# Performance work log

Measured on AMD Instinct MI355X. Metric: run time of the kernel, lower is better.

Reference implementation:

```python
import jax, jax.numpy as jnp
import numpy as np

T, B, D, H = 1024, 8, 1024, 16
HD = D // H  # head_dim = 64


def setup_inputs() -> dict:
    key = jax.random.key(0)
    ks = jax.random.split(key, 11)
    s = 1.0 / np.sqrt(D)
    return {
        "query": jax.random.normal(ks[0], (T, B, D), jnp.float32),
        "key": jax.random.normal(ks[1], (T, B, D), jnp.float32),
        "value": jax.random.normal(ks[2], (T, B, D), jnp.float32),
        "Wq": jax.random.normal(ks[3], (D, D), jnp.float32) * s,
        "bq": jax.random.normal(ks[4], (D,), jnp.float32) * s,
        "Wk": jax.random.normal(ks[5], (D, D), jnp.float32) * s,
        "bk": jax.random.normal(ks[6], (D,), jnp.float32) * s,
        "Wv": jax.random.normal(ks[7], (D, D), jnp.float32) * s,
        "bv": jax.random.normal(ks[8], (D,), jnp.float32) * s,
        "Wo": jax.random.normal(ks[9], (D, D), jnp.float32) * s,
        "bo": jax.random.normal(ks[10], (D,), jnp.float32) * s,
    }


def reference(query, key, value, Wq, bq, Wk, bk, Wv, bv, Wo, bo):
    # query/key/value: (T, B, D) seq-first, as in nn.MultiheadAttention
    t, b, d = query.shape
    scale = HD ** -0.5
    # projections (torch Linear: x @ W.T + b), split into heads -> (B, H, T, HD)
    q = (query @ Wq.T + bq).reshape(t, b, H, HD).transpose(1, 2, 0, 3)
    k = (key @ Wk.T + bk).reshape(t, b, H, HD).transpose(1, 2, 0, 3)
    v = (value @ Wv.T + bv).reshape(t, b, H, HD).transpose(1, 2, 0, 3)
    # full (B, H, T, T) scores, matching the module's explicit materialization
    attn = jnp.einsum('bhtd,bhsd->bhts', q, k) * scale
    attn = jax.nn.softmax(attn, axis=-1)
    # (B, H, T, HD) -> (T, B, D)
    out = jnp.einsum('bhts,bhsd->bhtd', attn, v)
    out = out.transpose(2, 0, 1, 3).reshape(t, b, d)
    return out @ Wo.T + bo
```

## Files before the change

kernel.cpp:

```cpp
#include <hip/hip_runtime.h>

#define T_SEQ 1024
#define BATCH 8
#define DMODEL 1024
#define NHEAD 16
#define HDIM 64
#define M_ROWS (T_SEQ * BATCH)

typedef unsigned short ushort_t;
typedef __attribute__((ext_vector_type(8))) short short8;
typedef __attribute__((ext_vector_type(4))) float f32x4;

#define G2L16(g, l) __builtin_amdgcn_global_load_lds(                      \
    (const __attribute__((address_space(1))) void*)(g),                    \
    (__attribute__((address_space(3))) void*)(l), 16, 0, 0)

static __device__ __forceinline__ ushort_t f2bf(float f) {
    unsigned int u = __builtin_bit_cast(unsigned int, f);
    u += 0x7FFFu + ((u >> 16) & 1u);
    return (ushort_t)(u >> 16);
}

__global__ __launch_bounds__(256) void cast_bf16(const float4* __restrict__ in,
                                                 uint2* __restrict__ out, int n4) {
    int i = blockIdx.x * 256 + threadIdx.x;
    if (i < n4) {
        float4 v = in[i];
        uint2 o;
        o.x = (unsigned)f2bf(v.x) | ((unsigned)f2bf(v.y) << 16);
        o.y = (unsigned)f2bf(v.z) | ((unsigned)f2bf(v.w) << 16);
        out[i] = o;
    }
}

template<bool OUT_BF16>
__global__ __launch_bounds__(256) void gemm_bt_mfma(
    const ushort_t* __restrict__ A, const ushort_t* __restrict__ Wb,
    const float* __restrict__ bias, void* __restrict__ Yv,
    int M, int N, int K, float scale)
{
    __shared__ ushort_t As[128 * 32];
    __shared__ ushort_t Bs[128 * 32];

    const int tid  = threadIdx.x;
    const int lane = tid & 63;
    const int quad = lane >> 4;
    const int l16  = lane & 15;
    const int w    = tid >> 6;
    const int wm   = w >> 1;
    const int wn   = w & 1;
    const int bn   = blockIdx.x;
    const int bm   = blockIdx.y;

    const int srow_in = lane >> 2;
    const int sch     = lane & 3;

    const f32x4 zero4 = {0.f, 0.f, 0.f, 0.f};
    f32x4 acc[4][4];
#pragma unroll
    for (int i = 0; i < 4; i++)
#pragma unroll
        for (int j = 0; j < 4; j++) acc[i][j] = zero4;

    const int fswz = (l16 >> 1) & 3;

    for (int k0 = 0; k0 < K; k0 += 32) {
        __syncthreads();
#pragma unroll
        for (int u = 0; u < 2; u++) {
            int seg = w * 2 + u;
            int row = seg * 16 + srow_in;
            int chs = sch ^ ((row >> 1) & 3);
            G2L16(&A [(size_t)(bm * 128 + row) * K + k0 + chs * 8],
                  (char*)As + seg * 1024);
            G2L16(&Wb[(size_t)(bn * 128 + row) * K + k0 + chs * 8],
                  (char*)Bs + seg * 1024);
        }
        __syncthreads();

        short8 af[4], bfr[4];
#pragma unroll
        for (int i = 0; i < 4; i++) {
            int row = wm * 64 + i * 16 + l16;
            af[i] = *(const short8*)&As[row * 32 + (quad ^ fswz) * 8];
        }
#pragma unroll
        for (int j = 0; j < 4; j++) {
            int row = wn * 64 + j * 16 + l16;
            bfr[j] = *(const short8*)&Bs[row * 32 + (quad ^ fswz) * 8];
        }
#pragma unroll
        for (int i = 0; i < 4; i++)
#pragma unroll
            for (int j = 0; j < 4; j++)
                acc[i][j] = __builtin_amdgcn_mfma_f32_16x16x32_bf16(
                    af[i], bfr[j], acc[i][j], 0, 0, 0);
    }

    float bj[4];
#pragma unroll
    for (int j = 0; j < 4; j++) bj[j] = bias[bn * 128 + wn * 64 + j * 16 + l16];
#pragma unroll
    for (int i = 0; i < 4; i++) {
#pragma unroll
        for (int r = 0; r < 4; r++) {
            size_t row = (size_t)(bm * 128 + wm * 64 + i * 16 + quad * 4 + r);
#pragma unroll
            for (int j = 0; j < 4; j++) {
                int col = bn * 128 + wn * 64 + j * 16 + l16;
                float v = (acc[i][j][r] + bj[j]) * scale;
                if (OUT_BF16) ((ushort_t*)Yv)[row * N + col] = f2bf(v);
                else          ((float*)   Yv)[row * N + col] = v;
            }
        }
    }
}

__global__ __launch_bounds__(256) void transpose_v(
    const ushort_t* __restrict__ Vp, ushort_t* __restrict__ Vt)
{
    __shared__ ushort_t Ts[64][72];
    const int tid = threadIdx.x;
    const int t0 = blockIdx.x * 64;
    const int bh = blockIdx.y;
    const int b = bh >> 4, h = bh & 15;

#pragma unroll
    for (int u = 0; u < 2; u++) {
        int e = u * 256 + tid;
        int row = e >> 3, ch = (e & 7) * 8;
        uint4 v = *(const uint4*)&Vp[((size_t)(t0 + row) * BATCH + b) * DMODEL + h * 64 + ch];
        *(uint4*)&Ts[row][ch] = v;
    }
    __syncthreads();
#pragma unroll
    for (int u = 0; u < 2; u++) {
        int e = u * 256 + tid;
        int d = e >> 3, tc = (e & 7) * 8;
        uint4 o;
        o.x = (unsigned)Ts[tc + 0][d] | ((unsigned)Ts[tc + 1][d] << 16);
        o.y = (unsigned)Ts[tc + 2][d] | ((unsigned)Ts[tc + 3][d] << 16);
        o.z = (unsigned)Ts[tc + 4][d] | ((unsigned)Ts[tc + 5][d] << 16);
        o.w = (unsigned)Ts[tc + 6][d] | ((unsigned)Ts[tc + 7][d] << 16);
        *(uint4*)&Vt[((size_t)(bh * 64 + d)) * T_SEQ + t0 + tc] = o;
    }
}

__global__ __launch_bounds__(256) void attn_mfma(
    const ushort_t* __restrict__ Qp, const ushort_t* __restrict__ Kp,
    const ushort_t* __restrict__ VtG, ushort_t* __restrict__ Ao)
{
    __shared__ ushort_t Ks[64 * 64];
    __shared__ ushort_t Vs[64 * 64];
    __shared__ ushort_t Pl[4][32][72];

    const int tid  = threadIdx.x;
    const int lane = tid & 63;
    const int w    = tid >> 6;
    const int quad = lane >> 4;
    const int l16  = lane & 15;
    const int bid  = blockIdx.x;
    const int qb   = bid >> 7;
    const int bh   = bid & 127;
    const int b    = bh >> 4, h = bh & 15;
    const int hoff = h * 64;
    const int q0   = qb * 128 + w * 32;

    const int srow_in = lane >> 3;
    const int sch     = lane & 7;

    short8 qf[2][2];
#pragma unroll
    for (int rt = 0; rt < 2; rt++)
#pragma unroll
        for (int ks = 0; ks < 2; ks++)
            qf[rt][ks] = *(const short8*)&Qp[((size_t)(q0 + rt * 16 + l16) * BATCH + b) * DMODEL
                                             + hoff + ks * 32 + quad * 8];

    short8 ones;
#pragma unroll
    for (int i = 0; i < 8; i++) ones[i] = (short)0x3F80;

    const f32x4 zero4 = {0.f, 0.f, 0.f, 0.f};
    f32x4 oacc[2][4], lacc[2];
#pragma unroll
    for (int rt = 0; rt < 2; rt++) {
        lacc[rt] = zero4;
#pragma unroll
        for (int c = 0; c < 4; c++) oacc[rt][c] = zero4;
    }

    for (int s0 = 0; s0 < T_SEQ; s0 += 64) {
        __syncthreads();
#pragma unroll
        for (int u = 0; u < 2; u++) {
            int seg = w * 2 + u;
            int row = seg * 8 + srow_in;
            int chs = sch ^ (row & 7);
            G2L16(&Kp[((size_t)(s0 + row) * BATCH + b) * DMODEL + hoff + chs * 8],
                  (char*)Ks + seg * 1024);
            G2L16(&VtG[((size_t)(bh * 64 + row)) * T_SEQ + s0 + chs * 8],
                  (char*)Vs + seg * 1024);
        }
        __syncthreads();

        f32x4 sacc[2][4];
#pragma unroll
        for (int rt = 0; rt < 2; rt++)
#pragma unroll
            for (int c = 0; c < 4; c++) sacc[rt][c] = zero4;
#pragma unroll
        for (int c = 0; c < 4; c++) {
            int row = c * 16 + l16;
#pragma unroll
            for (int ks = 0; ks < 2; ks++) {
                short8 kf = *(const short8*)&Ks[row * 64 + (((ks * 4 + quad) ^ (row & 7)) * 8)];
#pragma unroll
                for (int rt = 0; rt < 2; rt++)
                    sacc[rt][c] = __builtin_amdgcn_mfma_f32_16x16x32_bf16(
                        qf[rt][ks], kf, sacc[rt][c], 0, 0, 0);
            }
        }

#pragma unroll
        for (int rt = 0; rt < 2; rt++)
#pragma unroll
            for (int c = 0; c < 4; c++)
#pragma unroll
                for (int r = 0; r < 4; r++)
                    Pl[w][rt * 16 + quad * 4 + r][c * 16 + l16] =
                        f2bf(__expf(sacc[rt][c][r]));

        short8 pf[2][2];
#pragma unroll
        for (int rt = 0; rt < 2; rt++)
#pragma unroll
            for (int ks = 0; ks < 2; ks++)
                pf[rt][ks] = *(const short8*)&Pl[w][rt * 16 + l16][ks * 32 + quad * 8];

#pragma unroll
        for (int rt = 0; rt < 2; rt++)
#pragma unroll
            for (int ks = 0; ks < 2; ks++)
                lacc[rt] = __builtin_amdgcn_mfma_f32_16x16x32_bf16(
                    pf[rt][ks], ones, lacc[rt], 0, 0, 0);

#pragma unroll
        for (int dt = 0; dt < 4; dt++) {
            int row = dt * 16 + l16;
#pragma unroll
            for (int ks = 0; ks < 2; ks++) {
                short8 vf = *(const short8*)&Vs[row * 64 + (((ks * 4 + quad) ^ (row & 7)) * 8)];
#pragma unroll
                for (int rt = 0; rt < 2; rt++)
                    oacc[rt][dt] = __builtin_amdgcn_mfma_f32_16x16x32_bf16(
                        pf[rt][ks], vf, oacc[rt][dt], 0, 0, 0);
            }
        }
    }

#pragma unroll
    for (int rt = 0; rt < 2; rt++)
#pragma unroll
        for (int r = 0; r < 4; r++) {
            float inv = 1.f / lacc[rt][r];
            size_t t = (size_t)(q0 + rt * 16 + quad * 4 + r);
#pragma unroll
            for (int c = 0; c < 4; c++)
                Ao[(t * BATCH + b) * DMODEL + hoff + c * 16 + l16] =
                    f2bf(oacc[rt][c][r] * inv);
        }
}

extern "C" void kernel_launch(void* const* d_in, const int* in_sizes, int n_in,
                              void* d_out, int out_size, void* d_ws, size_t ws_size,
                              hipStream_t stream)
{
    const float* q  = (const float*)d_in[0];
    const float* k  = (const float*)d_in[1];
    const float* v  = (const float*)d_in[2];
    const float* Wq = (const float*)d_in[3];
    const float* bq = (const float*)d_in[4];
    const float* Wk = (const float*)d_in[5];
    const float* bk = (const float*)d_in[6];
    const float* Wv = (const float*)d_in[7];
    const float* bv = (const float*)d_in[8];
    const float* Wo = (const float*)d_in[9];
    const float* bo = (const float*)d_in[10];

    ushort_t* ws = (ushort_t*)d_ws;
    const size_t E = (size_t)M_ROWS * DMODEL;
    const size_t EW = (size_t)DMODEL * DMODEL;
    ushort_t* qb  = ws;
    ushort_t* kb  = ws + E;
    ushort_t* vb  = ws + 2 * E;
    ushort_t* Qp  = ws + 3 * E;
    ushort_t* Kp  = ws + 4 * E;
    ushort_t* Vp  = ws + 5 * E;
    ushort_t* Wqb = ws + 6 * E;
    ushort_t* Wkb = Wqb + EW;
    ushort_t* Wvb = Wkb + EW;
    ushort_t* Wob = Wvb + EW;
    ushort_t* Vt  = qb;
    ushort_t* Aob = kb;

    const int n4_in = (int)(E / 4);
    const int n4_w  = (int)(EW / 4);
    cast_bf16<<<n4_in / 256, 256, 0, stream>>>((const float4*)q,  (uint2*)qb,  n4_in);
    cast_bf16<<<n4_in / 256, 256, 0, stream>>>((const float4*)k,  (uint2*)kb,  n4_in);
    cast_bf16<<<n4_in / 256, 256, 0, stream>>>((const float4*)v,  (uint2*)vb,  n4_in);
    cast_bf16<<<n4_w  / 256, 256, 0, stream>>>((const float4*)Wq, (uint2*)Wqb, n4_w);
    cast_bf16<<<n4_w  / 256, 256, 0, stream>>>((const float4*)Wk, (uint2*)Wkb, n4_w);
    cast_bf16<<<n4_w  / 256, 256, 0, stream>>>((const float4*)Wv, (uint2*)Wvb, n4_w);
    cast_bf16<<<n4_w  / 256, 256, 0, stream>>>((const float4*)Wo, (uint2*)Wob, n4_w);

    dim3 gg(DMODEL / 128, M_ROWS / 128);
    gemm_bt_mfma<true><<<gg, 256, 0, stream>>>(qb, Wqb, bq, Qp, M_ROWS, DMODEL, DMODEL, 0.125f);
    gemm_bt_mfma<true><<<gg, 256, 0, stream>>>(kb, Wkb, bk, Kp, M_ROWS, DMODEL, DMODEL, 1.0f);
    gemm_bt_mfma<true><<<gg, 256, 0, stream>>>(vb, Wvb, bv, Vp, M_ROWS, DMODEL, DMODEL, 1.0f);

    transpose_v<<<dim3(T_SEQ / 64, BATCH * NHEAD), 256, 0, stream>>>(Vp, Vt);

    attn_mfma<<<dim3(8 * 128), 256, 0, stream>>>(Qp, Kp, Vt, Aob);

    gemm_bt_mfma<false><<<gg, 256, 0, stream>>>(Aob, Wob, bo, d_out, M_ROWS, DMODEL, DMODEL, 1.0f);
}
```

Measured before the change: 372.6 us.

## Batch cast kernels, use packed bf16 converts, transpose attention MFMA operands for vectorized stores

Merges the seven fp32-to-bf16 cast launches into two grid-batched launches and uses the hardware packed bf16 convert when it is available. In the attention kernel the MFMA operands are swapped so each lane holds four consecutive columns of a row. This lets P be written to LDS as packed 8-byte stores and the output be staged through LDS and written to global memory as 16-byte rows instead of scattered 2-byte stores. It also relies on the row-sum layout from the swapped ones-MFMA so that a single lacc element serves as the normalizer, which is a correctness-sensitive change.

```diff
diff --git a/kernel.cpp b/kernel.cpp
--- a/kernel.cpp
+++ b/kernel.cpp
@@ -21,16 +21,49 @@
     return (ushort_t)(u >> 16);
 }
 
-__global__ __launch_bounds__(256) void cast_bf16(const float4* __restrict__ in,
-                                                 uint2* __restrict__ out, int n4) {
+#if __has_builtin(__builtin_amdgcn_cvt_pk_bf16_f32)
+typedef __attribute__((ext_vector_type(2))) __bf16 bf16x2_t;
+static __device__ __forceinline__ unsigned pk2(float lo, float hi) {
+    bf16x2_t r = __builtin_amdgcn_cvt_pk_bf16_f32(lo, hi);
+    return __builtin_bit_cast(unsigned, r);
+}
+#else
+static __device__ __forceinline__ unsigned pk2(float lo, float hi) {
+    return (unsigned)f2bf(lo) | ((unsigned)f2bf(hi) << 16);
+}
+#endif
+
+__global__ __launch_bounds__(256) void cast3_bf16(
+    const float4* __restrict__ a, const float4* __restrict__ b,
+    const float4* __restrict__ c,
+    uint2* __restrict__ oa, uint2* __restrict__ ob, uint2* __restrict__ oc,
+    int n4)
+{
     int i = blockIdx.x * 256 + threadIdx.x;
-    if (i < n4) {
-        float4 v = in[i];
-        uint2 o;
-        o.x = (unsigned)f2bf(v.x) | ((unsigned)f2bf(v.y) << 16);
-        o.y = (unsigned)f2bf(v.z) | ((unsigned)f2bf(v.w) << 16);
-        out[i] = o;
-    }
+    if (i >= n4) return;
+    const float4* src = (blockIdx.y == 0) ? a : (blockIdx.y == 1) ? b : c;
+    uint2* dst        = (blockIdx.y == 0) ? oa : (blockIdx.y == 1) ? ob : oc;
+    float4 v = src[i];
+    uint2 o; o.x = pk2(v.x, v.y); o.y = pk2(v.z, v.w);
+    dst[i] = o;
+}
+
+__global__ __launch_bounds__(256) void cast4_bf16(
+    const float4* __restrict__ a, const float4* __restrict__ b,
+    const float4* __restrict__ c, const float4* __restrict__ d,
+    uint2* __restrict__ oa, uint2* __restrict__ ob,
+    uint2* __restrict__ oc, uint2* __restrict__ od,
+    int n4)
+{
+    int i = blockIdx.x * 256 + threadIdx.x;
+    if (i >= n4) return;
+    const float4* src = (blockIdx.y == 0) ? a : (blockIdx.y == 1) ? b
+                      : (blockIdx.y == 2) ? c : d;
+    uint2* dst        = (blockIdx.y == 0) ? oa : (blockIdx.y == 1) ? ob
+                      : (blockIdx.y == 2) ? oc : od;
+    float4 v = src[i];
+    uint2 o; o.x = pk2(v.x, v.y); o.y = pk2(v.z, v.w);
+    dst[i] = o;
 }
 
 template<bool OUT_BF16>
@@ -218,18 +251,19 @@
 #pragma unroll
                 for (int rt = 0; rt < 2; rt++)
                     sacc[rt][c] = __builtin_amdgcn_mfma_f32_16x16x32_bf16(
-                        qf[rt][ks], kf, sacc[rt][c], 0, 0, 0);
+                        kf, qf[rt][ks], sacc[rt][c], 0, 0, 0);
             }
         }
 
 #pragma unroll
         for (int rt = 0; rt < 2; rt++)
 #pragma unroll
-            for (int c = 0; c < 4; c++)
-#pragma unroll
-                for (int r = 0; r < 4; r++)
-                    Pl[w][rt * 16 + quad * 4 + r][c * 16 + l16] =
-                        f2bf(__expf(sacc[rt][c][r]));
+            for (int c = 0; c < 4; c++) {
+                uint2 pv;
+                pv.x = pk2(__expf(sacc[rt][c][0]), __expf(sacc[rt][c][1]));
+                pv.y = pk2(__expf(sacc[rt][c][2]), __expf(sacc[rt][c][3]));
+                *(uint2*)&Pl[w][rt * 16 + l16][c * 16 + quad * 4] = pv;
+            }
 
         short8 pf[2][2];
 #pragma unroll
@@ -243,7 +277,7 @@
 #pragma unroll
             for (int ks = 0; ks < 2; ks++)
                 lacc[rt] = __builtin_amdgcn_mfma_f32_16x16x32_bf16(
-                    pf[rt][ks], ones, lacc[rt], 0, 0, 0);
+                    ones, pf[rt][ks], lacc[rt], 0, 0, 0);
 
 #pragma unroll
         for (int dt = 0; dt < 4; dt++) {
@@ -254,22 +288,29 @@
 #pragma unroll
                 for (int rt = 0; rt < 2; rt++)
                     oacc[rt][dt] = __builtin_amdgcn_mfma_f32_16x16x32_bf16(
-                        pf[rt][ks], vf, oacc[rt][dt], 0, 0, 0);
+                        vf, pf[rt][ks], oacc[rt][dt], 0, 0, 0);
             }
         }
     }
 
 #pragma unroll
-    for (int rt = 0; rt < 2; rt++)
-#pragma unroll
-        for (int r = 0; r < 4; r++) {
-            float inv = 1.f / lacc[rt][r];
-            size_t t = (size_t)(q0 + rt * 16 + quad * 4 + r);
-#pragma unroll
-            for (int c = 0; c < 4; c++)
-                Ao[(t * BATCH + b) * DMODEL + hoff + c * 16 + l16] =
-                    f2bf(oacc[rt][c][r] * inv);
-        }
+    for (int rt = 0; rt < 2; rt++) {
+        float inv = 1.f / lacc[rt][0];
+#pragma unroll
+        for (int dt = 0; dt < 4; dt++) {
+            uint2 ov;
+            ov.x = pk2(oacc[rt][dt][0] * inv, oacc[rt][dt][1] * inv);
+            ov.y = pk2(oacc[rt][dt][2] * inv, oacc[rt][dt][3] * inv);
+            *(uint2*)&Pl[w][rt * 16 + l16][dt * 16 + quad * 4] = ov;
+        }
+    }
+#pragma unroll
+    for (int it = 0; it < 4; it++) {
+        int row = it * 8 + (lane >> 3);
+        int ch  = lane & 7;
+        uint4 val = *(const uint4*)&Pl[w][row][ch * 8];
+        *(uint4*)&Ao[((size_t)(q0 + row) * BATCH + b) * DMODEL + hoff + ch * 8] = val;
+    }
 }
 
 extern "C" void kernel_launch(void* const* d_in, const int* in_sizes, int n_in,
@@ -306,13 +347,12 @@
 
     const int n4_in = (int)(E / 4);
     const int n4_w  = (int)(EW / 4);
-    cast_bf16<<<n4_in / 256, 256, 0, stream>>>((const float4*)q,  (uint2*)qb,  n4_in);
-    cast_bf16<<<n4_in / 256, 256, 0, stream>>>((const float4*)k,  (uint2*)kb,  n4_in);
-    cast_bf16<<<n4_in / 256, 256, 0, stream>>>((const float4*)v,  (uint2*)vb,  n4_in);
-    cast_bf16<<<n4_w  / 256, 256, 0, stream>>>((const float4*)Wq, (uint2*)Wqb, n4_w);
-    cast_bf16<<<n4_w  / 256, 256, 0, stream>>>((const float4*)Wk, (uint2*)Wkb, n4_w);
-    cast_bf16<<<n4_w  / 256, 256, 0, stream>>>((const float4*)Wv, (uint2*)Wvb, n4_w);
-    cast_bf16<<<n4_w  / 256, 256, 0, stream>>>((const float4*)Wo, (uint2*)Wob, n4_w);
+    cast3_bf16<<<dim3(n4_in / 256, 3), 256, 0, stream>>>(
+        (const float4*)q, (const float4*)k, (const float4*)v,
+        (uint2*)qb, (uint2*)kb, (uint2*)vb, n4_in);
+    cast4_bf16<<<dim3(n4_w / 256, 4), 256, 0, stream>>>(
+        (const float4*)Wq, (const float4*)Wk, (const float4*)Wv, (const float4*)Wo,
+        (uint2*)Wqb, (uint2*)Wkb, (uint2*)Wvb, (uint2*)Wob, n4_w);
 
     dim3 gg(DMODEL / 128, M_ROWS / 128);
     gemm_bt_mfma<true><<<gg, 256, 0, stream>>>(qb, Wqb, bq, Qp, M_ROWS, DMODEL, DMODEL, 0.125f);
```

New measurement: 355.1 us. 4.7% less time.
